# Performance work log

Hardware: AMD Instinct MI355X
Metric: run time of the kernel (lower is better)

## Reference

```python
import jax, jax.numpy as jnp
import numpy as np

B, C, H, W, D, V = 1, 32, 128, 160, 48, 3


def _make_proj_matrices():
    # K @ [R|t] per view, small rotations/baselines so warps land mostly in-bounds
    K = np.array([[400.0, 0.0, 80.0], [0.0, 400.0, 64.0], [0.0, 0.0, 1.0]])
    mats = []
    for v in range(V):
        a = 0.04 * v
        R = np.array([[np.cos(a), 0.0, np.sin(a)], [0.0, 1.0, 0.0], [-np.sin(a), 0.0, np.cos(a)]])
        t = np.array([120.0 * v, 0.0, 0.0])  # baseline in mm, consistent with depth ~425..935
        P = np.eye(4)
        P[:3, :3] = K @ R
        P[:3, 3] = K @ t
        mats.append(P)
    return jnp.asarray(np.stack(mats)[None], dtype=jnp.float32)  # [1,V,4,4]


def setup_inputs() -> dict:
    key = jax.random.key(0)
    k0, k1, k2, kw = jax.random.split(key, 4)
    feat0 = jax.random.normal(k0, (B, C, H, W), jnp.float32)
    feat1 = jax.random.normal(k1, (B, C, H, W), jnp.float32)
    feat2 = jax.random.normal(k2, (B, C, H, W), jnp.float32)
    depth_values = jnp.broadcast_to(
        jnp.linspace(425.0, 935.0, D, dtype=jnp.float32)[None], (B, D))
    w_reg = jax.random.normal(kw, (1, C, 3, 3, 3), jnp.float32) * 0.05
    b_reg = jnp.zeros((1,), jnp.float32)
    return dict(feat0=feat0, feat1=feat1, feat2=feat2,
                proj_matrices=_make_proj_matrices(),
                depth_values=depth_values, w_reg=w_reg, b_reg=b_reg,
                num_depth=D)


def _bilinear_sample(fea, gx, gy):
    # fea: [C,H,W]; gx,gy: [N] pixel coords (align_corners=True convention),
    # zero padding outside image (matches F.grid_sample padding_mode='zeros').
    h, w = fea.shape[1], fea.shape[2]
    x0 = jnp.floor(gx)
    y0 = jnp.floor(gy)
    wx = gx - x0
    wy = gy - y0

    def corner(xi, yi, wgt):
        valid = ((xi >= 0) & (xi <= w - 1) & (yi >= 0) & (yi <= h - 1)).astype(fea.dtype)
        xc = jnp.clip(xi, 0, w - 1).astype(jnp.int32)
        yc = jnp.clip(yi, 0, h - 1).astype(jnp.int32)
        return fea[:, yc, xc] * (wgt * valid)[None]  # [C,N]

    return (corner(x0, y0, (1 - wx) * (1 - wy)) +
            corner(x0 + 1, y0, wx * (1 - wy)) +
            corner(x0, y0 + 1, (1 - wx) * wy) +
            corner(x0 + 1, y0 + 1, wx * wy))


def homo_warping(src_fea, src_proj, ref_proj, depth_values):
    # src_fea [B,C,H,W], projs [B,4,4], depth_values [B,D] -> [B,C,D,H,W]
    b, c, h, w = src_fea.shape
    d = depth_values.shape[1]
    proj = src_proj @ jnp.linalg.inv(ref_proj)
    rot = proj[:, :3, :3]           # [B,3,3]
    trans = proj[:, :3, 3]          # [B,3]
    yy, xx = jnp.meshgrid(jnp.arange(h, dtype=src_fea.dtype),
                          jnp.arange(w, dtype=src_fea.dtype), indexing='ij')
    xyz = jnp.stack([xx.ravel(), yy.ravel(), jnp.ones(h * w, src_fea.dtype)], 0)  # [3,HW]
    rot_xyz = jnp.einsum('bij,jn->bin', rot, xyz)                                  # [B,3,HW]
    p = rot_xyz[:, :, None, :] * depth_values[:, None, :, None] + trans[:, :, None, None]  # [B,3,D,HW]
    z = p[:, 2]
    gx = (p[:, 0] / z).reshape(b, -1)  # [B, D*HW]
    gy = (p[:, 1] / z).reshape(b, -1)
    warped = jax.vmap(_bilinear_sample)(src_fea, gx, gy)  # [B,C,D*HW]
    return warped.reshape(b, c, d, h, w)


def reference(feat0, feat1, feat2, proj_matrices, depth_values, w_reg, b_reg, num_depth):
    features = [feat0, feat1, feat2]
    projs = [proj_matrices[:, v] for v in range(proj_matrices.shape[1])]
    ref_fea, ref_proj = features[0], projs[0]
    num_views = len(features)
    b, c, h, w = ref_fea.shape

    ref_volume = jnp.broadcast_to(ref_fea[:, :, None], (b, c, num_depth, h, w))
    volume_sum = ref_volume
    volume_sq_sum = ref_volume ** 2
    for src_fea, src_proj in zip(features[1:], projs[1:]):
        wv = homo_warping(src_fea, src_proj, ref_proj, depth_values)
        volume_sum = volume_sum + wv
        volume_sq_sum = volume_sq_sum + wv * wv

    volume_variance = volume_sq_sum / num_views - (volume_sum / num_views) ** 2

    # cost_regularization stand-in: 3D conv C -> 1, SAME padding, then squeeze channel
    cost = jax.lax.conv_general_dilated(
        volume_variance, w_reg, window_strides=(1, 1, 1), padding='SAME',
        dimension_numbers=('NCDHW', 'OIDHW', 'NCDHW'))
    cost = cost[:, 0] + b_reg[0]            # [B,D,H,W]

    prob_volume = jax.nn.softmax(cost, axis=1)
    depth = jnp.sum(prob_volume * depth_values[:, :, None, None], axis=1)  # [B,H,W]
    photometric_confidence = jnp.max(prob_volume, axis=1)                   # [B,H,W]
    return depth, photometric_confidence
```

## Files before the change

### kernel.cpp

```cpp
#include <hip/hip_runtime.h>
#include <hip/hip_fp16.h>
#include <math.h>

#define Cc 32
#define Hc 128
#define Wc 160
#define Dc 48
#define HWc (Hc*Wc)
#define TS 16
#define HALO (TS+2)
#define NPOS (HALO*HALO)
#define DCHUNK 4
#define NCHUNK (Dc/DCHUNK)
#define VSTR4 5
#define NPASS 6


typedef _Float16 h8v __attribute__((ext_vector_type(8)));
typedef float f32x4 __attribute__((ext_vector_type(4)));

union F4H { float4 f; __half2 h[4]; };
union PackCW { __half2 h[4]; float4 f; };
union AF { float4 f; h8v h; };

__global__ void k_pre(const float* __restrict__ f0, const float* __restrict__ f1,
                      const float* __restrict__ f2, const float* __restrict__ proj,
                      const float* __restrict__ wreg,
                      _Float16* __restrict__ o0, _Float16* __restrict__ o1, _Float16* __restrict__ o2,
                      float* __restrict__ wsproj, _Float16* __restrict__ w2h,
                      float* __restrict__ costvol) {
    const int tid = threadIdx.x;
    const int p = blockIdx.x * 256 + tid;
    if (blockIdx.y == 3) {
        if (p < HWc) {
#pragma unroll
            for (int d = 0; d < Dc; d++) costvol[d * HWc + p] = 0.f;
        }
        return;
    }
    if (p < HWc) {
        const float* f = (blockIdx.y == 0) ? f0 : (blockIdx.y == 1) ? f1 : f2;
        _Float16*    o = (blockIdx.y == 0) ? o0 : (blockIdx.y == 1) ? o1 : o2;
        float v[Cc];
#pragma unroll
        for (int c = 0; c < Cc; c++) v[c] = f[c * HWc + p];
        union { __half2 h[16]; float4 f4[4]; } rec;
#pragma unroll
        for (int c = 0; c < 16; c++) rec.h[c] = __floats2half2_rn(v[2 * c], v[2 * c + 1]);
        float4* o4 = (float4*)(o + (size_t)p * Cc);
#pragma unroll
        for (int j = 0; j < 4; j++) o4[j] = rec.f4[j];
    }
    if (blockIdx.x == 0 && blockIdx.y == 0) {
        for (int i = tid; i < 9 * 3 * Cc; i += 256) {
            int ch = i & 31;
            int t  = i >> 5;
            int kd = t % 3;
            int khkw = t / 3;
            w2h[i] = (_Float16)wreg[ch * 27 + kd * 9 + khkw];
        }
        if (tid == 0) {
            float a[4][8];
            for (int i = 0; i < 4; i++)
                for (int j = 0; j < 4; j++) {
                    a[i][j]     = proj[i * 4 + j];
                    a[i][j + 4] = (i == j) ? 1.f : 0.f;
                }
            for (int col = 0; col < 4; col++) {
                int piv = col; float best = fabsf(a[col][col]);
                for (int r = col + 1; r < 4; r++) {
                    float v = fabsf(a[r][col]);
                    if (v > best) { best = v; piv = r; }
                }
                if (piv != col)
                    for (int j = 0; j < 8; j++) { float t = a[col][j]; a[col][j] = a[piv][j]; a[piv][j] = t; }
                float inv = 1.f / a[col][col];
                for (int j = 0; j < 8; j++) a[col][j] *= inv;
                for (int r = 0; r < 4; r++) if (r != col) {
                    float f = a[r][col];
                    for (int j = 0; j < 8; j++) a[r][j] -= f * a[col][j];
                }
            }
            for (int v = 1; v < 3; v++) {
                const float* P = proj + v * 16;
                float M[3][4];
                for (int i = 0; i < 3; i++)
                    for (int j = 0; j < 4; j++) {
                        float s = 0.f;
                        for (int k = 0; k < 4; k++) s += P[i * 4 + k] * a[k][4 + j];
                        M[i][j] = s;
                    }
                float* o = wsproj + (v - 1) * 12;
                o[0] = M[0][0]; o[1] = M[0][1]; o[2] = M[0][2];
                o[3] = M[1][0]; o[4] = M[1][1]; o[5] = M[1][2];
                o[6] = M[2][0]; o[7] = M[2][1]; o[8] = M[2][2];
                o[9] = M[0][3]; o[10] = M[1][3]; o[11] = M[2][3];
            }
        }
    }
}

__global__ __launch_bounds__(256, 2) void k_cost(
    const _Float16* __restrict__ fT0, const _Float16* __restrict__ fT1,
    const _Float16* __restrict__ fT2, const float* __restrict__ dvals,
    const float4* __restrict__ w2h4, const float* __restrict__ wsproj,
    float* __restrict__ costvol)
{
    __shared__ float4 var_l[NPOS * VSTR4];
    __shared__ float4 parW[NPOS];
    __shared__ float4 cost_l4[6 * 64];
    __shared__ float projl[24];

    float* cost_l = (float*)cost_l4;

    const int tid = threadIdx.x;
    if (tid < 24) projl[tid] = wsproj[tid];
#pragma unroll
    for (int i = 0; i < 6; i++) cost_l[i * 256 + tid] = 0.f;
    __syncthreads();

    const int tileX = blockIdx.x;
    const int tileY = blockIdx.y;
    const int d0    = blockIdx.z * DCHUNK;
    const int baseH = tileY * TS - 1, baseW = tileX * TS - 1;

    const int posq = tid >> 2;
    const int cc   = tid & 3;

    const int wid  = tid >> 6;
    const int lane = tid & 63;
    const int lrow = lane & 15;
    const int lsel = lane >> 4;

    const float4* fT0_4 = (const float4*)fT0;
    const float4* fT1_4 = (const float4*)fT1;
    const float4* fT2_4 = (const float4*)fT2;

    h8v bfr[9];
    {
        const int kdc = (lrow < 3) ? lrow : 0;
#pragma unroll
        for (int t = 0; t < 9; t++) {
            AF u; u.f = w2h4[(t * 3 + kdc) * 4 + lsel];
            bfr[t] = u.h;
        }
    }

    float rAx[2][2], rAy[2][2], rAz[2][2];
    float trn[2][3];
#pragma unroll
    for (int v = 0; v < 2; v++) {
        trn[v][0] = projl[v * 12 + 9];
        trn[v][1] = projl[v * 12 + 10];
        trn[v][2] = projl[v * 12 + 11];
    }
    int amask = 0;
#pragma unroll
    for (int s = 0; s < 2; s++) {
        int p = tid + s * 256;
        bool act = p < NPOS;
        int pp = act ? p : 0;
        int py = pp / HALO, px = pp % HALO;
        int hyi = baseH + py, hxi = baseW + px;
        bool ok = act && hyi >= 0 && hyi < Hc && hxi >= 0 && hxi < Wc;
        if (ok) amask |= (1 << s);
        float hx = (float)hxi, hy = (float)hyi;
#pragma unroll
        for (int v = 0; v < 2; v++) {
            const float* R = projl + v * 12;
            rAx[s][v] = fmaf(R[0], hx, fmaf(R[1], hy, R[2]));
            rAy[s][v] = fmaf(R[3], hx, fmaf(R[4], hy, R[5]));
            rAz[s][v] = fmaf(R[6], hx, fmaf(R[7], hy, R[8]));
        }
    }

    int    bmask = 0;
    float4 rfv[NPASS];
#pragma unroll
    for (int s = 0; s < NPASS; s++) {
        int p = posq + s * 64;
        bool act = p < NPOS;
        int pp = act ? p : 0;
        int py = pp / HALO, px = pp % HALO;
        int hyi = baseH + py, hxi = baseW + px;
        bool ok = act && hyi >= 0 && hyi < Hc && hxi >= 0 && hxi < Wc;
        if (ok) bmask |= (1 << s);
        rfv[s] = ok ? fT0_4[(hyi * Wc + hxi) * 4 + cc] : make_float4(0.f, 0.f, 0.f, 0.f);
    }

    auto phaseA = [&](int dpn) {
        const float depthN = dvals[dpn];
#pragma unroll
        for (int s = 0; s < 2; s++) {
            int p = tid + s * 256;
            if (p >= NPOS) break;
            if (!((amask >> s) & 1)) continue;
            float cw[2][4]; unsigned int pk[4];
#pragma unroll
            for (int v = 0; v < 2; v++) {
                float X = fmaf(rAx[s][v], depthN, trn[v][0]);
                float Y = fmaf(rAy[s][v], depthN, trn[v][1]);
                float Z = fmaf(rAz[s][v], depthN, trn[v][2]);
                float iz = 1.f / Z;
                float gx = X * iz, gy = Y * iz;
                float x0f = floorf(gx), y0f = floorf(gy);
                float wx = gx - x0f, wy = gy - y0f;
                int x0 = (int)x0f, y0 = (int)y0f;
                bool vx0 = (x0 >= 0) & (x0 <= Wc - 1);
                bool vx1 = (x0 + 1 >= 0) & (x0 + 1 <= Wc - 1);
                bool vy0 = (y0 >= 0) & (y0 <= Hc - 1);
                bool vy1 = (y0 + 1 >= 0) & (y0 + 1 <= Hc - 1);
                int xc0 = min(max(x0, 0), Wc - 1), xc1 = min(max(x0 + 1, 0), Wc - 1);
                int yc0 = min(max(y0, 0), Hc - 1), yc1 = min(max(y0 + 1, 0), Hc - 1);
                float ax = 1.f - wx, ay = 1.f - wy;
                cw[v][0] = (vx0 && vy0) ? ax * ay : 0.f;
                cw[v][1] = (vx1 && vy0) ? wx * ay : 0.f;
                cw[v][2] = (vx0 && vy1) ? ax * wy : 0.f;
                cw[v][3] = (vx1 && vy1) ? wx * wy : 0.f;
                unsigned int i0 = (unsigned int)(yc0 * Wc + xc0);
                unsigned int i1 = (unsigned int)(yc0 * Wc + xc1);
                unsigned int i2 = (unsigned int)(yc1 * Wc + xc0);
                unsigned int i3 = (unsigned int)(yc1 * Wc + xc1);
                pk[v * 2 + 0] = i0 | (i1 << 16);
                pk[v * 2 + 1] = i2 | (i3 << 16);
            }
            PackCW pc;
            pc.h[0] = __floats2half2_rn(cw[0][0], cw[0][1]);
            pc.h[1] = __floats2half2_rn(cw[0][2], cw[0][3]);
            pc.h[2] = __floats2half2_rn(cw[1][0], cw[1][1]);
            pc.h[3] = __floats2half2_rn(cw[1][2], cw[1][3]);
            parW[p] = pc.f;
            var_l[p * VSTR4 + 4] = make_float4(__uint_as_float(pk[0]), __uint_as_float(pk[1]),
                                               __uint_as_float(pk[2]), __uint_as_float(pk[3]));
        }
    };

    const int dpFirst = d0;
    const int dpLast  = d0 + DCHUNK - 1;

    phaseA(dpFirst);
    __syncthreads();

    const __half2 kT3 = __float2half2_rn(1.f / 3.f);
    const __half2 kN9 = __float2half2_rn(-1.f / 9.f);

    for (int dp = dpFirst; dp <= dpLast; dp++) {
#pragma unroll
        for (int s = 0; s < NPASS; s++) {
            int p = posq + s * 64;
            if (p >= NPOS) continue;
            const int vaddr = p * VSTR4 + cc;
            if (!((bmask >> s) & 1)) {
                var_l[vaddr] = make_float4(0.f, 0.f, 0.f, 0.f);
                continue;
            }
            PackCW pc; pc.f = parW[p];
            float4 pkf = var_l[p * VSTR4 + 4];
            __half2 c0a = __low2half2(pc.h[0]), c0b = __high2half2(pc.h[0]);
            __half2 c0c = __low2half2(pc.h[1]), c0d = __high2half2(pc.h[1]);
            __half2 c1a = __low2half2(pc.h[2]), c1b = __high2half2(pc.h[2]);
            __half2 c1c = __low2half2(pc.h[3]), c1d = __high2half2(pc.h[3]);
            unsigned int u0 = __float_as_uint(pkf.x), u1 = __float_as_uint(pkf.y);
            unsigned int u2 = __float_as_uint(pkf.z), u3 = __float_as_uint(pkf.w);
            int i00 = u0 & 0xffff, i01 = u0 >> 16, i02 = u1 & 0xffff, i03 = u1 >> 16;
            int i10 = u2 & 0xffff, i11 = u2 >> 16, i12 = u3 & 0xffff, i13 = u3 >> 16;
            F4H rf; rf.f = rfv[s];
            F4H t00, t01, t10, t11, u00v, u01v, u10v, u11v, vo;
            t00.f = fT1_4[i00 * 4 + cc];
            t01.f = fT1_4[i01 * 4 + cc];
            t10.f = fT1_4[i02 * 4 + cc];
            t11.f = fT1_4[i03 * 4 + cc];
            u00v.f = fT2_4[i10 * 4 + cc];
            u01v.f = fT2_4[i11 * 4 + cc];
            u10v.f = fT2_4[i12 * 4 + cc];
            u11v.f = fT2_4[i13 * 4 + cc];
#pragma unroll
            for (int j = 0; j < 4; j++) {
                __half2 a1 = __hfma2(c0a, t00.h[j], __hfma2(c0b, t01.h[j],
                             __hfma2(c0c, t10.h[j], __hmul2(c0d, t11.h[j]))));
                __half2 a2 = __hfma2(c1a, u00v.h[j], __hfma2(c1b, u01v.h[j],
                             __hfma2(c1c, u10v.h[j], __hmul2(c1d, u11v.h[j]))));
                __half2 r  = rf.h[j];
                __half2 sm = __hadd2(r, __hadd2(a1, a2));
                __half2 sq = __hfma2(r, r, __hfma2(a1, a1, __hmul2(a2, a2)));
                vo.h[j] = __hfma2(__hmul2(sm, sm), kN9, __hmul2(sq, kT3));
            }
            var_l[vaddr] = vo.f;
        }
        __syncthreads();

        if (dp < dpLast) phaseA(dp + 1);

#pragma unroll
        for (int g = 0; g < 4; g++) {
            const int R = (wid << 2) + g;
            f32x4 acc = {0.f, 0.f, 0.f, 0.f};
#pragma unroll
            for (int t = 0; t < 9; t++) {
                const int dy = t / 3, dx = t % 3;
                AF a; a.f = var_l[((R + dy) * HALO + dx + lrow) * VSTR4 + lsel];
                acc = __builtin_amdgcn_mfma_f32_16x16x32_f16(a.h, bfr[t], acc, 0, 0, 0);
            }
            if (lrow < 3) {
                const int idx = ((dp - d0) + 2 - lrow) * 64 + R * 4 + lsel;
                float4 c = cost_l4[idx];
                c.x += acc[0]; c.y += acc[1]; c.z += acc[2]; c.w += acc[3];
                cost_l4[idx] = c;
            }
        }
        __syncthreads();
    }

    const int gy = tileY * TS + (tid >> 4), gx = tileX * TS + (tid & 15);
    float* cbase = costvol + gy * Wc + gx;
#pragma unroll
    for (int slot = 0; slot < 6; slot++) {
        const int s = d0 + slot - 1;
        if (s >= 0 && s < Dc)
            atomicAdd(cbase + (size_t)s * HWc, cost_l[slot * 256 + tid]);
    }
}

__global__ void k_softmax(const float* __restrict__ costvol, const float* __restrict__ dvals,
                          const float* __restrict__ breg, float* __restrict__ out)
{
    const int px = blockIdx.x * 256 + threadIdx.x;
    if (px >= HWc) return;
    const float bias = breg[0];
    float c[Dc];
    float m = -1e30f;
#pragma unroll
    for (int d = 0; d < Dc; d++) {
        c[d] = costvol[d * HWc + px] + bias;
        m = fmaxf(m, c[d]);
    }
    float se = 0.f, sed = 0.f, me = 0.f;
#pragma unroll
    for (int d = 0; d < Dc; d++) {
        float e = __expf(c[d] - m);
        se += e;
        sed = fmaf(e, dvals[d], sed);
        me = fmaxf(me, e);
    }
    float inv = 1.f / se;
    out[px]       = sed * inv;
    out[HWc + px] = me * inv;
}

extern "C" void kernel_launch(void* const* d_in, const int* in_sizes, int n_in,
                              void* d_out, int out_size, void* d_ws, size_t ws_size,
                              hipStream_t stream) {
    const float* f0    = (const float*)d_in[0];
    const float* f1    = (const float*)d_in[1];
    const float* f2    = (const float*)d_in[2];
    const float* proj  = (const float*)d_in[3];
    const float* dvals = (const float*)d_in[4];
    const float* wreg  = (const float*)d_in[5];
    const float* breg  = (const float*)d_in[6];

    float* ws      = (float*)d_ws;
    float* wsproj  = ws;
    _Float16* w2h  = (_Float16*)(ws + 32);
    _Float16* fT0h = (_Float16*)(ws + 32 + 432);
    _Float16* fT1h = fT0h + (size_t)HWc * Cc;
    _Float16* fT2h = fT1h + (size_t)HWc * Cc;
    float* costvol = (float*)(fT2h + (size_t)HWc * Cc);

    k_pre<<<dim3((HWc + 255) / 256, 4), 256, 0, stream>>>(f0, f1, f2, proj, wreg,
                                                          fT0h, fT1h, fT2h, wsproj, w2h,
                                                          costvol);

    dim3 grid(Wc / TS, Hc / TS, NCHUNK);
    k_cost<<<grid, 256, 0, stream>>>(fT0h, fT1h, fT2h, dvals, (const float4*)w2h,
                                     wsproj, costvol);

    k_softmax<<<(HWc + 255) / 256, 256, 0, stream>>>(costvol, dvals, breg, (float*)d_out);
}
```

Before: 121.3 us.

## Software-pipeline warp sampling with conv via double-buffered variance tiles

Removes the separate phase-A pass that stored bilinear weights and indices in shared memory. Each thread now computes projections per pass in registers and issues gathers two passes ahead, interleaved with the MFMA conv on the previous depth, using a double-buffered variance tile. DCHUNK rises from 4 to 6 to cut halo and atomic overhead per depth, and launch bounds drop to 1 block per CU. This raises register pressure and lowers occupancy in exchange for overlapping gather latency with the conv.

New measurement: 154.4 us. +27.3%, slower.

```diff
diff --git a/kernel.cpp b/kernel.cpp
--- a/kernel.cpp
+++ b/kernel.cpp
@@ -10,10 +10,10 @@
 #define TS 16
 #define HALO (TS+2)
 #define NPOS (HALO*HALO)
-#define DCHUNK 4
+#define DCHUNK 6
 #define NCHUNK (Dc/DCHUNK)
-#define VSTR4 5
 #define NPASS 6
+#define NSLOT (DCHUNK+2)
 
 
 typedef _Float16 h8v __attribute__((ext_vector_type(8)));
@@ -100,23 +100,21 @@
     }
 }
 
-__global__ __launch_bounds__(256, 2) void k_cost(
+__global__ __launch_bounds__(256, 1) void k_cost(
     const _Float16* __restrict__ fT0, const _Float16* __restrict__ fT1,
     const _Float16* __restrict__ fT2, const float* __restrict__ dvals,
     const float4* __restrict__ w2h4, const float* __restrict__ wsproj,
     float* __restrict__ costvol)
 {
-    __shared__ float4 var_l[NPOS * VSTR4];
-    __shared__ float4 parW[NPOS];
-    __shared__ float4 cost_l4[6 * 64];
+    __shared__ float4 var_l[2][NPOS * 4];
+    __shared__ float4 cost_l4[NSLOT * 64];
     __shared__ float projl[24];
-
     float* cost_l = (float*)cost_l4;
 
     const int tid = threadIdx.x;
     if (tid < 24) projl[tid] = wsproj[tid];
 #pragma unroll
-    for (int i = 0; i < 6; i++) cost_l[i * 256 + tid] = 0.f;
+    for (int i = 0; i < NSLOT; i++) cost_l[i * 256 + tid] = 0.f;
     __syncthreads();
 
     const int tileX = blockIdx.x;
@@ -146,7 +144,9 @@
         }
     }
 
-    float rAx[2][2], rAy[2][2], rAz[2][2];
+    float rx[NPASS][2], ry[NPASS][2], rz[NPASS][2];
+    int   ref_i[NPASS];
+    int   bmask = 0;
     float trn[2][3];
 #pragma unroll
     for (int v = 0; v < 2; v++) {
@@ -154,28 +154,6 @@
         trn[v][1] = projl[v * 12 + 10];
         trn[v][2] = projl[v * 12 + 11];
     }
-    int amask = 0;
-#pragma unroll
-    for (int s = 0; s < 2; s++) {
-        int p = tid + s * 256;
-        bool act = p < NPOS;
-        int pp = act ? p : 0;
-        int py = pp / HALO, px = pp % HALO;
-        int hyi = baseH + py, hxi = baseW + px;
-        bool ok = act && hyi >= 0 && hyi < Hc && hxi >= 0 && hxi < Wc;
-        if (ok) amask |= (1 << s);
-        float hx = (float)hxi, hy = (float)hyi;
-#pragma unroll
-        for (int v = 0; v < 2; v++) {
-            const float* R = projl + v * 12;
-            rAx[s][v] = fmaf(R[0], hx, fmaf(R[1], hy, R[2]));
-            rAy[s][v] = fmaf(R[3], hx, fmaf(R[4], hy, R[5]));
-            rAz[s][v] = fmaf(R[6], hx, fmaf(R[7], hy, R[8]));
-        }
-    }
-
-    int    bmask = 0;
-    float4 rfv[NPASS];
 #pragma unroll
     for (int s = 0; s < NPASS; s++) {
         int p = posq + s * 64;
@@ -185,128 +163,141 @@
         int hyi = baseH + py, hxi = baseW + px;
         bool ok = act && hyi >= 0 && hyi < Hc && hxi >= 0 && hxi < Wc;
         if (ok) bmask |= (1 << s);
-        rfv[s] = ok ? fT0_4[(hyi * Wc + hxi) * 4 + cc] : make_float4(0.f, 0.f, 0.f, 0.f);
-    }
-
-    auto phaseA = [&](int dpn) {
-        const float depthN = dvals[dpn];
-#pragma unroll
-        for (int s = 0; s < 2; s++) {
-            int p = tid + s * 256;
-            if (p >= NPOS) break;
-            if (!((amask >> s) & 1)) continue;
-            float cw[2][4]; unsigned int pk[4];
-#pragma unroll
-            for (int v = 0; v < 2; v++) {
-                float X = fmaf(rAx[s][v], depthN, trn[v][0]);
-                float Y = fmaf(rAy[s][v], depthN, trn[v][1]);
-                float Z = fmaf(rAz[s][v], depthN, trn[v][2]);
-                float iz = 1.f / Z;
-                float gx = X * iz, gy = Y * iz;
-                float x0f = floorf(gx), y0f = floorf(gy);
-                float wx = gx - x0f, wy = gy - y0f;
-                int x0 = (int)x0f, y0 = (int)y0f;
-                bool vx0 = (x0 >= 0) & (x0 <= Wc - 1);
-                bool vx1 = (x0 + 1 >= 0) & (x0 + 1 <= Wc - 1);
-                bool vy0 = (y0 >= 0) & (y0 <= Hc - 1);
-                bool vy1 = (y0 + 1 >= 0) & (y0 + 1 <= Hc - 1);
-                int xc0 = min(max(x0, 0), Wc - 1), xc1 = min(max(x0 + 1, 0), Wc - 1);
-                int yc0 = min(max(y0, 0), Hc - 1), yc1 = min(max(y0 + 1, 0), Hc - 1);
-                float ax = 1.f - wx, ay = 1.f - wy;
-                cw[v][0] = (vx0 && vy0) ? ax * ay : 0.f;
-                cw[v][1] = (vx1 && vy0) ? wx * ay : 0.f;
-                cw[v][2] = (vx0 && vy1) ? ax * wy : 0.f;
-                cw[v][3] = (vx1 && vy1) ? wx * wy : 0.f;
-                unsigned int i0 = (unsigned int)(yc0 * Wc + xc0);
-                unsigned int i1 = (unsigned int)(yc0 * Wc + xc1);
-                unsigned int i2 = (unsigned int)(yc1 * Wc + xc0);
-                unsigned int i3 = (unsigned int)(yc1 * Wc + xc1);
-                pk[v * 2 + 0] = i0 | (i1 << 16);
-                pk[v * 2 + 1] = i2 | (i3 << 16);
-            }
-            PackCW pc;
-            pc.h[0] = __floats2half2_rn(cw[0][0], cw[0][1]);
-            pc.h[1] = __floats2half2_rn(cw[0][2], cw[0][3]);
-            pc.h[2] = __floats2half2_rn(cw[1][0], cw[1][1]);
-            pc.h[3] = __floats2half2_rn(cw[1][2], cw[1][3]);
-            parW[p] = pc.f;
-            var_l[p * VSTR4 + 4] = make_float4(__uint_as_float(pk[0]), __uint_as_float(pk[1]),
-                                               __uint_as_float(pk[2]), __uint_as_float(pk[3]));
-        }
+        ref_i[s] = (ok ? (hyi * Wc + hxi) : 0) * 4 + cc;
+        float hx = (float)hxi, hy = (float)hyi;
+#pragma unroll
+        for (int v = 0; v < 2; v++) {
+            const float* R = projl + v * 12;
+            rx[s][v] = fmaf(R[0], hx, fmaf(R[1], hy, R[2]));
+            ry[s][v] = fmaf(R[3], hx, fmaf(R[4], hy, R[5]));
+            rz[s][v] = fmaf(R[6], hx, fmaf(R[7], hy, R[8]));
+        }
+    }
+
+    struct Flight {
+        float4 rf, t00, t01, t10, t11, u00, u01, u10, u11;
+        float4 pcf;
     };
-
-    const int dpFirst = d0;
-    const int dpLast  = d0 + DCHUNK - 1;
-
-    phaseA(dpFirst);
-    __syncthreads();
 
     const __half2 kT3 = __float2half2_rn(1.f / 3.f);
     const __half2 kN9 = __float2half2_rn(-1.f / 9.f);
 
-    for (int dp = dpFirst; dp <= dpLast; dp++) {
-#pragma unroll
-        for (int s = 0; s < NPASS; s++) {
-            int p = posq + s * 64;
-            if (p >= NPOS) continue;
-            const int vaddr = p * VSTR4 + cc;
-            if (!((bmask >> s) & 1)) {
-                var_l[vaddr] = make_float4(0.f, 0.f, 0.f, 0.f);
-                continue;
-            }
-            PackCW pc; pc.f = parW[p];
-            float4 pkf = var_l[p * VSTR4 + 4];
-            __half2 c0a = __low2half2(pc.h[0]), c0b = __high2half2(pc.h[0]);
-            __half2 c0c = __low2half2(pc.h[1]), c0d = __high2half2(pc.h[1]);
-            __half2 c1a = __low2half2(pc.h[2]), c1b = __high2half2(pc.h[2]);
-            __half2 c1c = __low2half2(pc.h[3]), c1d = __high2half2(pc.h[3]);
-            unsigned int u0 = __float_as_uint(pkf.x), u1 = __float_as_uint(pkf.y);
-            unsigned int u2 = __float_as_uint(pkf.z), u3 = __float_as_uint(pkf.w);
-            int i00 = u0 & 0xffff, i01 = u0 >> 16, i02 = u1 & 0xffff, i03 = u1 >> 16;
-            int i10 = u2 & 0xffff, i11 = u2 >> 16, i12 = u3 & 0xffff, i13 = u3 >> 16;
-            F4H rf; rf.f = rfv[s];
-            F4H t00, t01, t10, t11, u00v, u01v, u10v, u11v, vo;
-            t00.f = fT1_4[i00 * 4 + cc];
-            t01.f = fT1_4[i01 * 4 + cc];
-            t10.f = fT1_4[i02 * 4 + cc];
-            t11.f = fT1_4[i03 * 4 + cc];
-            u00v.f = fT2_4[i10 * 4 + cc];
-            u01v.f = fT2_4[i11 * 4 + cc];
-            u10v.f = fT2_4[i12 * 4 + cc];
-            u11v.f = fT2_4[i13 * 4 + cc];
-#pragma unroll
-            for (int j = 0; j < 4; j++) {
-                __half2 a1 = __hfma2(c0a, t00.h[j], __hfma2(c0b, t01.h[j],
-                             __hfma2(c0c, t10.h[j], __hmul2(c0d, t11.h[j]))));
-                __half2 a2 = __hfma2(c1a, u00v.h[j], __hfma2(c1b, u01v.h[j],
-                             __hfma2(c1c, u10v.h[j], __hmul2(c1d, u11v.h[j]))));
-                __half2 r  = rf.h[j];
-                __half2 sm = __hadd2(r, __hadd2(a1, a2));
-                __half2 sq = __hfma2(r, r, __hfma2(a1, a1, __hmul2(a2, a2)));
-                vo.h[j] = __hfma2(__hmul2(sm, sm), kN9, __hmul2(sq, kT3));
-            }
-            var_l[vaddr] = vo.f;
-        }
-        __syncthreads();
-
-        if (dp < dpLast) phaseA(dp + 1);
-
-#pragma unroll
-        for (int g = 0; g < 4; g++) {
-            const int R = (wid << 2) + g;
-            f32x4 acc = {0.f, 0.f, 0.f, 0.f};
-#pragma unroll
-            for (int t = 0; t < 9; t++) {
-                const int dy = t / 3, dx = t % 3;
-                AF a; a.f = var_l[((R + dy) * HALO + dx + lrow) * VSTR4 + lsel];
-                acc = __builtin_amdgcn_mfma_f32_16x16x32_f16(a.h, bfr[t], acc, 0, 0, 0);
-            }
-            if (lrow < 3) {
-                const int idx = ((dp - d0) + 2 - lrow) * 64 + R * 4 + lsel;
-                float4 c = cost_l4[idx];
-                c.x += acc[0]; c.y += acc[1]; c.z += acc[2]; c.w += acc[3];
-                cost_l4[idx] = c;
-            }
+    auto issue = [&](int s, float depthN, Flight& F) {
+        const bool ok = (bmask >> s) & 1;
+        float cw[2][4]; int idx[2][4];
+#pragma unroll
+        for (int v = 0; v < 2; v++) {
+            float X = fmaf(rx[s][v], depthN, trn[v][0]);
+            float Y = fmaf(ry[s][v], depthN, trn[v][1]);
+            float Z = fmaf(rz[s][v], depthN, trn[v][2]);
+            float iz = 1.f / Z;
+            float gx = X * iz, gy = Y * iz;
+            float x0f = floorf(gx), y0f = floorf(gy);
+            float wx = gx - x0f, wy = gy - y0f;
+            int x0 = (int)x0f, y0 = (int)y0f;
+            bool vx0 = (x0 >= 0) & (x0 <= Wc - 1);
+            bool vx1 = (x0 >= -1) & (x0 <= Wc - 2);
+            bool vy0 = (y0 >= 0) & (y0 <= Hc - 1);
+            bool vy1 = (y0 >= -1) & (y0 <= Hc - 2);
+            int xc0 = min(max(x0, 0), Wc - 1), xc1 = min(max(x0 + 1, 0), Wc - 1);
+            int yc0 = min(max(y0, 0), Hc - 1), yc1 = min(max(y0 + 1, 0), Hc - 1);
+            float ax = 1.f - wx, ay = 1.f - wy;
+            cw[v][0] = (vx0 && vy0 && ok) ? ax * ay : 0.f;
+            cw[v][1] = (vx1 && vy0 && ok) ? wx * ay : 0.f;
+            cw[v][2] = (vx0 && vy1 && ok) ? ax * wy : 0.f;
+            cw[v][3] = (vx1 && vy1 && ok) ? wx * wy : 0.f;
+            idx[v][0] = (yc0 * Wc + xc0) * 4 + cc;
+            idx[v][1] = (yc0 * Wc + xc1) * 4 + cc;
+            idx[v][2] = (yc1 * Wc + xc0) * 4 + cc;
+            idx[v][3] = (yc1 * Wc + xc1) * 4 + cc;
+        }
+        PackCW pc;
+        pc.h[0] = __floats2half2_rn(cw[0][0], cw[0][1]);
+        pc.h[1] = __floats2half2_rn(cw[0][2], cw[0][3]);
+        pc.h[2] = __floats2half2_rn(cw[1][0], cw[1][1]);
+        pc.h[3] = __floats2half2_rn(cw[1][2], cw[1][3]);
+        F.pcf = pc.f;
+        F.rf  = fT0_4[ref_i[s]];
+        F.t00 = fT1_4[idx[0][0]]; F.t01 = fT1_4[idx[0][1]];
+        F.t10 = fT1_4[idx[0][2]]; F.t11 = fT1_4[idx[0][3]];
+        F.u00 = fT2_4[idx[1][0]]; F.u01 = fT2_4[idx[1][1]];
+        F.u10 = fT2_4[idx[1][2]]; F.u11 = fT2_4[idx[1][3]];
+    };
+
+    auto finish = [&](int s, Flight& F, int nxt) {
+        const bool ok = (bmask >> s) & 1;
+        PackCW pc; pc.f = F.pcf;
+        __half2 c0a = __low2half2(pc.h[0]), c0b = __high2half2(pc.h[0]);
+        __half2 c0c = __low2half2(pc.h[1]), c0d = __high2half2(pc.h[1]);
+        __half2 c1a = __low2half2(pc.h[2]), c1b = __high2half2(pc.h[2]);
+        __half2 c1c = __low2half2(pc.h[3]), c1d = __high2half2(pc.h[3]);
+        F4H rf; rf.f = ok ? F.rf : make_float4(0.f, 0.f, 0.f, 0.f);
+        F4H t00, t01, t10, t11, u00, u01, u10, u11, vo;
+        t00.f = F.t00; t01.f = F.t01; t10.f = F.t10; t11.f = F.t11;
+        u00.f = F.u00; u01.f = F.u01; u10.f = F.u10; u11.f = F.u11;
+#pragma unroll
+        for (int j = 0; j < 4; j++) {
+            __half2 a1 = __hfma2(c0a, t00.h[j], __hfma2(c0b, t01.h[j],
+                         __hfma2(c0c, t10.h[j], __hmul2(c0d, t11.h[j]))));
+            __half2 a2 = __hfma2(c1a, u00.h[j], __hfma2(c1b, u01.h[j],
+                         __hfma2(c1c, u10.h[j], __hmul2(c1d, u11.h[j]))));
+            __half2 r  = rf.h[j];
+            __half2 sm = __hadd2(r, __hadd2(a1, a2));
+            __half2 sq = __hfma2(r, r, __hfma2(a1, a1, __hmul2(a2, a2)));
+            vo.h[j] = __hfma2(__hmul2(sm, sm), kN9, __hmul2(sq, kT3));
+        }
+        int p = posq + s * 64;
+        if (p < NPOS) var_l[nxt][p * 4 + cc] = vo.f;
+    };
+
+    auto conv_g = [&](int g, int cur, int dp) {
+        const int R = (wid << 2) + g;
+        f32x4 acc = {0.f, 0.f, 0.f, 0.f};
+#pragma unroll
+        for (int t = 0; t < 9; t++) {
+            const int dy = t / 3, dx = t % 3;
+            AF a; a.f = var_l[cur][((R + dy) * HALO + dx + lrow) * 4 + lsel];
+            acc = __builtin_amdgcn_mfma_f32_16x16x32_f16(a.h, bfr[t], acc, 0, 0, 0);
+        }
+        if (lrow < 3) {
+            const int idx = ((dp - d0) + 2 - lrow) * 64 + R * 4 + lsel;
+            float4 c = cost_l4[idx];
+            c.x += acc[0]; c.y += acc[1]; c.z += acc[2]; c.w += acc[3];
+            cost_l4[idx] = c;
+        }
+    };
+
+    {
+        const float dN = dvals[d0];
+        Flight fa, fb;
+        issue(0, dN, fa); issue(1, dN, fb);
+        finish(0, fa, 0); issue(2, dN, fa);
+        finish(1, fb, 0); issue(3, dN, fb);
+        finish(2, fa, 0); issue(4, dN, fa);
+        finish(3, fb, 0); issue(5, dN, fb);
+        finish(4, fa, 0); finish(5, fb, 0);
+    }
+    __syncthreads();
+
+    const int dpLast = d0 + DCHUNK - 1;
+    for (int dp = d0; dp <= dpLast; dp++) {
+        const int cur = (dp - d0) & 1, nxt = cur ^ 1;
+        if (dp < dpLast) {
+            const float dN = dvals[dp + 1];
+            Flight fa, fb;
+            issue(0, dN, fa); issue(1, dN, fb);
+            conv_g(0, cur, dp);
+            finish(0, fa, nxt); issue(2, dN, fa);
+            conv_g(1, cur, dp);
+            finish(1, fb, nxt); issue(3, dN, fb);
+            conv_g(2, cur, dp);
+            finish(2, fa, nxt); issue(4, dN, fa);
+            conv_g(3, cur, dp);
+            finish(3, fb, nxt); issue(5, dN, fb);
+            finish(4, fa, nxt); finish(5, fb, nxt);
+        } else {
+            conv_g(0, cur, dp); conv_g(1, cur, dp);
+            conv_g(2, cur, dp); conv_g(3, cur, dp);
         }
         __syncthreads();
     }
@@ -314,7 +305,7 @@
     const int gy = tileY * TS + (tid >> 4), gx = tileX * TS + (tid & 15);
     float* cbase = costvol + gy * Wc + gx;
 #pragma unroll
-    for (int slot = 0; slot < 6; slot++) {
+    for (int slot = 0; slot < NSLOT; slot++) {
         const int s = d0 + slot - 1;
         if (s >= 0 && s < Dc)
             atomicAdd(cbase + (size_t)s * HWc, cost_l[slot * 256 + tid]);
```

## Double-buffer variance tiles, swizzle LDS layout, and double depth chunk

Applied to the files above, without the earlier changes.

Splits the variance buffer into two ping-pong LDS buffers so that warping/variance for the next depth plane can be computed while the MFMA conv consumes the previous one. It moves the packed indices into their own array and replaces the padded stride-5 layout with an XOR swizzle to avoid bank conflicts. It also raises DCHUNK from 4 to 8, so there are fewer blocks, fewer halo slots, and fewer atomics relative to useful work. The cost is more LDS per block, which may lower occupancy, and fewer blocks in the grid.

Measured after the change: 123.3 us. No clear change (+1.6%).

```diff
diff --git a/kernel.cpp b/kernel.cpp
--- a/kernel.cpp
+++ b/kernel.cpp
@@ -10,10 +10,10 @@
 #define TS 16
 #define HALO (TS+2)
 #define NPOS (HALO*HALO)
-#define DCHUNK 4
+#define DCHUNK 8
 #define NCHUNK (Dc/DCHUNK)
-#define VSTR4 5
 #define NPASS 6
+#define NSLOT (DCHUNK+2)
 
 
 typedef _Float16 h8v __attribute__((ext_vector_type(8)));
@@ -106,17 +106,18 @@
     const float4* __restrict__ w2h4, const float* __restrict__ wsproj,
     float* __restrict__ costvol)
 {
-    __shared__ float4 var_l[NPOS * VSTR4];
+    __shared__ float4 varA[NPOS * 4];
+    __shared__ float4 varB[NPOS * 4];
     __shared__ float4 parW[NPOS];
-    __shared__ float4 cost_l4[6 * 64];
+    __shared__ float4 parI[NPOS];
+    __shared__ float4 cost_l4[NSLOT * 64];
     __shared__ float projl[24];
-
     float* cost_l = (float*)cost_l4;
 
     const int tid = threadIdx.x;
     if (tid < 24) projl[tid] = wsproj[tid];
 #pragma unroll
-    for (int i = 0; i < 6; i++) cost_l[i * 256 + tid] = 0.f;
+    for (int i = 0; i < NSLOT; i++) cost_l[i * 256 + tid] = 0.f;
     __syncthreads();
 
     const int tileX = blockIdx.x;
@@ -230,32 +231,26 @@
             pc.h[2] = __floats2half2_rn(cw[1][0], cw[1][1]);
             pc.h[3] = __floats2half2_rn(cw[1][2], cw[1][3]);
             parW[p] = pc.f;
-            var_l[p * VSTR4 + 4] = make_float4(__uint_as_float(pk[0]), __uint_as_float(pk[1]),
-                                               __uint_as_float(pk[2]), __uint_as_float(pk[3]));
+            parI[p] = make_float4(__uint_as_float(pk[0]), __uint_as_float(pk[1]),
+                                  __uint_as_float(pk[2]), __uint_as_float(pk[3]));
         }
     };
-
-    const int dpFirst = d0;
-    const int dpLast  = d0 + DCHUNK - 1;
-
-    phaseA(dpFirst);
-    __syncthreads();
 
     const __half2 kT3 = __float2half2_rn(1.f / 3.f);
     const __half2 kN9 = __float2half2_rn(-1.f / 9.f);
 
-    for (int dp = dpFirst; dp <= dpLast; dp++) {
+    auto phaseB = [&](float4* dst) {
 #pragma unroll
         for (int s = 0; s < NPASS; s++) {
             int p = posq + s * 64;
             if (p >= NPOS) continue;
-            const int vaddr = p * VSTR4 + cc;
+            const int vaddr = (p << 2) + (cc ^ ((p >> 1) & 3));
             if (!((bmask >> s) & 1)) {
-                var_l[vaddr] = make_float4(0.f, 0.f, 0.f, 0.f);
+                dst[vaddr] = make_float4(0.f, 0.f, 0.f, 0.f);
                 continue;
             }
             PackCW pc; pc.f = parW[p];
-            float4 pkf = var_l[p * VSTR4 + 4];
+            float4 pkf = parI[p];
             __half2 c0a = __low2half2(pc.h[0]), c0b = __high2half2(pc.h[0]);
             __half2 c0c = __low2half2(pc.h[1]), c0d = __high2half2(pc.h[1]);
             __half2 c1a = __low2half2(pc.h[2]), c1b = __high2half2(pc.h[2]);
@@ -285,12 +280,11 @@
                 __half2 sq = __hfma2(r, r, __hfma2(a1, a1, __hmul2(a2, a2)));
                 vo.h[j] = __hfma2(__hmul2(sm, sm), kN9, __hmul2(sq, kT3));
             }
-            var_l[vaddr] = vo.f;
-        }
-        __syncthreads();
-
-        if (dp < dpLast) phaseA(dp + 1);
-
+            dst[vaddr] = vo.f;
+        }
+    };
+
+    auto conv = [&](const float4* src, int dp) {
 #pragma unroll
         for (int g = 0; g < 4; g++) {
             const int R = (wid << 2) + g;
@@ -298,7 +292,8 @@
 #pragma unroll
             for (int t = 0; t < 9; t++) {
                 const int dy = t / 3, dx = t % 3;
-                AF a; a.f = var_l[((R + dy) * HALO + dx + lrow) * VSTR4 + lsel];
+                const int pos = (R + dy) * HALO + dx + lrow;
+                AF a; a.f = src[(pos << 2) + (lsel ^ ((pos >> 1) & 3))];
                 acc = __builtin_amdgcn_mfma_f32_16x16x32_f16(a.h, bfr[t], acc, 0, 0, 0);
             }
             if (lrow < 3) {
@@ -308,13 +303,39 @@
                 cost_l4[idx] = c;
             }
         }
+    };
+
+    const int dpLast = d0 + DCHUNK - 1;
+
+    phaseA(d0);
+    __syncthreads();
+    phaseB(varA);
+    __syncthreads();
+    phaseA(d0 + 1);
+    __syncthreads();
+
+    for (int i = 0; i < DCHUNK / 2; i++) {
+        const int t = d0 + 2 * i;
+        phaseB(varB);
+        conv(varA, t);
         __syncthreads();
+        if (t + 2 <= dpLast) {
+            phaseA(t + 2);
+            __syncthreads();
+        }
+        if (t + 2 <= dpLast) phaseB(varA);
+        conv(varB, t + 1);
+        __syncthreads();
+        if (t + 3 <= dpLast) {
+            phaseA(t + 3);
+            __syncthreads();
+        }
     }
 
     const int gy = tileY * TS + (tid >> 4), gx = tileX * TS + (tid & 15);
     float* cbase = costvol + gy * Wc + gx;
 #pragma unroll
-    for (int slot = 0; slot < 6; slot++) {
+    for (int slot = 0; slot < NSLOT; slot++) {
         const int s = d0 + slot - 1;
         if (s >= 0 && s < Dc)
             atomicAdd(cbase + (size_t)s * HWc, cost_l[slot * 256 + tid]);
```
